# Optimization experiments

Measured on AMD Instinct MI355X. Metric: run time of the kernel, lower is better.

The kernel has to match this reference:

```python
import jax, jax.numpy as jnp
import numpy as np

N = 50000      # nodes
E = 800000     # edges (before self loops)
D_IN = 128
HID = 64
HEADS = 8
D_OUT = 10


def setup_inputs() -> dict:
    key = jax.random.key(0)
    ks = jax.random.split(key, 16)
    sc = 0.05
    x = jax.random.normal(ks[0], (N, D_IN), dtype=jnp.float32)
    edge_index = jax.random.randint(ks[1], (2, E), 0, N, dtype=jnp.int64)
    return {
        "x": x,
        "edge_index": edge_index,
        "W1": jax.random.normal(ks[2], (HEADS * HID, D_IN), dtype=jnp.float32) * sc,
        "a1_src": jax.random.normal(ks[3], (HEADS, HID), dtype=jnp.float32) * sc,
        "a1_dst": jax.random.normal(ks[4], (HEADS, HID), dtype=jnp.float32) * sc,
        "b1": jnp.zeros((HEADS * HID,), jnp.float32),
        "W2": jax.random.normal(ks[5], (HID, HEADS * HID), dtype=jnp.float32) * sc,
        "a2_src": jax.random.normal(ks[6], (1, HID), dtype=jnp.float32) * sc,
        "a2_dst": jax.random.normal(ks[7], (1, HID), dtype=jnp.float32) * sc,
        "b2": jnp.zeros((HID,), jnp.float32),
        "W3": jax.random.normal(ks[8], (HID, HID), dtype=jnp.float32) * sc,
        "a3_src": jax.random.normal(ks[9], (1, HID), dtype=jnp.float32) * sc,
        "a3_dst": jax.random.normal(ks[10], (1, HID), dtype=jnp.float32) * sc,
        "b3": jnp.zeros((HID,), jnp.float32),
        "Wc": jax.random.normal(ks[11], (D_OUT, HID), dtype=jnp.float32) * sc,
        "bc": jnp.zeros((D_OUT,), jnp.float32),
    }


def gat_conv(x, src, dst, W, a_src, a_dst, b, concat):
    """PyG GATConv (eval mode, add_self_loops already applied to src/dst)."""
    heads, out_ch = a_src.shape
    n = x.shape[0]
    h = (x @ W.T).reshape(n, heads, out_ch)          # [N, H, C]
    a_s = jnp.einsum('nhc,hc->nh', h, a_src)          # [N, H]
    a_d = jnp.einsum('nhc,hc->nh', h, a_dst)          # [N, H]
    e = jax.nn.leaky_relu(a_s[src] + a_d[dst], 0.2)   # [Etot, H]
    # segment softmax over incoming edges of each destination node
    m = jax.ops.segment_max(e, dst, num_segments=n)
    ex = jnp.exp(e - m[dst])
    s = jax.ops.segment_sum(ex, dst, num_segments=n)
    alpha = ex / (s[dst] + 1e-16)                     # [Etot, H]
    out = jax.ops.segment_sum(h[src] * alpha[:, :, None], dst, num_segments=n)
    if concat:
        out = out.reshape(n, heads * out_ch)
    else:
        out = out.mean(axis=1)
    return out + b


def reference(x, edge_index, W1, a1_src, a1_dst, b1, W2, a2_src, a2_dst, b2,
              W3, a3_src, a3_dst, b3, Wc, bc):
    loops = jnp.arange(N, dtype=edge_index.dtype)
    src = jnp.concatenate([edge_index[0], loops])
    dst = jnp.concatenate([edge_index[1], loops])
    h = jax.nn.elu(gat_conv(x, src, dst, W1, a1_src, a1_dst, b1, True))
    h = jax.nn.elu(gat_conv(h, src, dst, W2, a2_src, a2_dst, b2, False))
    h = jax.nn.elu(gat_conv(h, src, dst, W3, a3_src, a3_dst, b3, False))
    return h @ Wc.T + bc
```

## Files before the change

kernel.cpp:

```cpp
#include <hip/hip_runtime.h>
#include <math.h>

#define N_NODES 50000
#define N_EDGES 800000
#define ETOT    (N_EDGES + N_NODES)

typedef short bf16x8 __attribute__((ext_vector_type(8)));
typedef float f32x4  __attribute__((ext_vector_type(4)));

__device__ __forceinline__ float b2f(unsigned int u16) {
    return __uint_as_float(u16 << 16);
}
__device__ __forceinline__ unsigned short f2b(float f) {
    unsigned int u = __float_as_uint(f);
    u += 0x7fffu + ((u >> 16) & 1u);
    return (unsigned short)(u >> 16);
}
__device__ __forceinline__ void unpack8(uint4 v, float* f) {
    f[0] = __uint_as_float(v.x << 16); f[1] = __uint_as_float(v.x & 0xffff0000u);
    f[2] = __uint_as_float(v.y << 16); f[3] = __uint_as_float(v.y & 0xffff0000u);
    f[4] = __uint_as_float(v.z << 16); f[5] = __uint_as_float(v.z & 0xffff0000u);
    f[6] = __uint_as_float(v.w << 16); f[7] = __uint_as_float(v.w & 0xffff0000u);
}

__global__ void k_detect(const int* __restrict__ idx, int* __restrict__ flag) {
    int i = blockIdx.x * blockDim.x + threadIdx.x;
    int v = idx[2 * i + 1];
    unsigned long long any = __ballot(v != 0);
    if ((threadIdx.x & 63) == 0 && any) atomicOr(flag, 1);
}

__device__ __forceinline__ int edge_src(const int* idx, int e, int is32) {
    return is32 ? idx[e] : idx[2 * e];
}
__device__ __forceinline__ int edge_dst(const int* idx, int e, int is32) {
    return is32 ? idx[N_EDGES + e] : idx[2 * (N_EDGES + e)];
}

__global__ void k_degree(const int* __restrict__ idx, const int* __restrict__ flag,
                         int* __restrict__ deg) {
    int e = blockIdx.x * blockDim.x + threadIdx.x;
    if (e >= ETOT) return;
    int is32 = *flag;
    int d = (e < N_EDGES) ? edge_dst(idx, e, is32) : (e - N_EDGES);
    atomicAdd(&deg[d], 1);
}

__global__ __launch_bounds__(256) void k_scan1(const int* __restrict__ deg,
                                               int* __restrict__ rowptr,
                                               int* __restrict__ bsum) {
    __shared__ int sd[256];
    int t = threadIdx.x;
    int i = blockIdx.x * 256 + t;
    int v = (i < N_NODES) ? deg[i] : 0;
    sd[t] = v;
    __syncthreads();
#pragma unroll
    for (int off = 1; off < 256; off <<= 1) {
        int a = (t >= off) ? sd[t - off] : 0;
        __syncthreads();
        sd[t] += a;
        __syncthreads();
    }
    if (i < N_NODES) rowptr[i] = sd[t] - v;
    if (t == 255) bsum[blockIdx.x] = sd[255];
}

__global__ __launch_bounds__(256) void k_scan2(int* __restrict__ bsum,
                                               int* __restrict__ boff,
                                               int* __restrict__ rowptr,
                                               int nb) {
    __shared__ int sd[256];
    int t = threadIdx.x;
    int v = (t < nb) ? bsum[t] : 0;
    sd[t] = v;
    __syncthreads();
#pragma unroll
    for (int off = 1; off < 256; off <<= 1) {
        int a = (t >= off) ? sd[t - off] : 0;
        __syncthreads();
        sd[t] += a;
        __syncthreads();
    }
    boff[t] = sd[t] - v;
    if (t == 255) rowptr[N_NODES] = sd[255];
}

__global__ __launch_bounds__(256) void k_scan3(int* __restrict__ rowptr,
                                               const int* __restrict__ boff,
                                               int* __restrict__ cursor) {
    int i = blockIdx.x * 256 + threadIdx.x;
    if (i >= N_NODES) return;
    int r = rowptr[i] + boff[blockIdx.x];
    rowptr[i] = r;
    cursor[i] = r;
}

__global__ void k_scatter(const int* __restrict__ idx, const int* __restrict__ flag,
                          int* __restrict__ cursor, int* __restrict__ col) {
    int e = blockIdx.x * blockDim.x + threadIdx.x;
    if (e >= ETOT) return;
    int is32 = *flag;
    int s, d;
    if (e < N_EDGES) { s = edge_src(idx, e, is32); d = edge_dst(idx, e, is32); }
    else             { s = d = e - N_EDGES; }
    int pos = atomicAdd(&cursor[d], 1);
    col[pos] = s;
}

__global__ void k_cast_w(const float* __restrict__ w1, const float* __restrict__ w2,
                         const float* __restrict__ w3,
                         unsigned short* __restrict__ o1, unsigned short* __restrict__ o2,
                         unsigned short* __restrict__ o3) {
    int i = blockIdx.x * blockDim.x + threadIdx.x;
    if (i < 512 * 128 / 4) {
        float4 v = ((const float4*)w1)[i];
        ushort2* o = (ushort2*)(o1 + i * 4);
        o[0] = make_ushort2(f2b(v.x), f2b(v.y));
        o[1] = make_ushort2(f2b(v.z), f2b(v.w));
    }
    if (i < 64 * 512 / 4) {
        float4 v = ((const float4*)w2)[i];
        ushort2* o = (ushort2*)(o2 + i * 4);
        o[0] = make_ushort2(f2b(v.x), f2b(v.y));
        o[1] = make_ushort2(f2b(v.z), f2b(v.w));
    }
    if (i < 64 * 64 / 4) {
        float4 v = ((const float4*)w3)[i];
        ushort2* o = (ushort2*)(o3 + i * 4);
        o[0] = make_ushort2(f2b(v.x), f2b(v.y));
        o[1] = make_ushort2(f2b(v.z), f2b(v.w));
    }
}

template<int AFP32>
__global__ __launch_bounds__(256) void k_gemm(const float* __restrict__ Af,
                                              const unsigned short* __restrict__ Ab,
                                              const unsigned short* __restrict__ W,
                                              unsigned short* __restrict__ C,
                                              const float* __restrict__ a_src,
                                              const float* __restrict__ a_dst,
                                              float* __restrict__ asb,
                                              float* __restrict__ adb,
                                              int M, int K, int Nout, int Hstr) {
    __shared__ unsigned short As[64 * 40];
    __shared__ unsigned short Bs[64 * 40];
    __shared__ float red_s[4][64];
    __shared__ float red_d[4][64];
    int t = threadIdx.x;
    int w = t >> 6, l = t & 63;
    int quad = l >> 4, lm = l & 15;
    int m0 = blockIdx.y * 64, n0 = blockIdx.x * 64;
    int hd = blockIdx.x;
    int lr = t >> 2;
    int lc = (t & 3) * 8;

    f32x4 acc[4];
#pragma unroll
    for (int r = 0; r < 4; ++r) acc[r] = (f32x4){0.f, 0.f, 0.f, 0.f};

    for (int k0 = 0; k0 < K; k0 += 32) {
        int m = m0 + lr;
        if (AFP32) {
            float4 a0 = {0.f,0.f,0.f,0.f}, a1 = {0.f,0.f,0.f,0.f};
            if (m < M) {
                const float4* ap = (const float4*)(Af + (size_t)m * K + k0 + lc);
                a0 = ap[0]; a1 = ap[1];
            }
            unsigned int u0 = (unsigned int)f2b(a0.x) | ((unsigned int)f2b(a0.y) << 16);
            unsigned int u1 = (unsigned int)f2b(a0.z) | ((unsigned int)f2b(a0.w) << 16);
            unsigned int u2 = (unsigned int)f2b(a1.x) | ((unsigned int)f2b(a1.y) << 16);
            unsigned int u3 = (unsigned int)f2b(a1.z) | ((unsigned int)f2b(a1.w) << 16);
            *(uint4*)&As[lr * 40 + lc] = make_uint4(u0, u1, u2, u3);
        } else {
            uint4 av = make_uint4(0, 0, 0, 0);
            if (m < M) av = *(const uint4*)(Ab + (size_t)m * K + k0 + lc);
            *(uint4*)&As[lr * 40 + lc] = av;
        }
        uint4 bv = *(const uint4*)(W + (size_t)(n0 + lr) * K + k0 + lc);
        *(uint4*)&Bs[lr * 40 + lc] = bv;
        __syncthreads();

        bf16x8 bfrag = *(const bf16x8*)&Bs[(w * 16 + lm) * 40 + quad * 8];
#pragma unroll
        for (int r = 0; r < 4; ++r) {
            bf16x8 afrag = *(const bf16x8*)&As[(r * 16 + lm) * 40 + quad * 8];
            acc[r] = __builtin_amdgcn_mfma_f32_16x16x32_bf16(afrag, bfrag, acc[r], 0, 0, 0);
        }
        __syncthreads();
    }

#pragma unroll
    for (int r = 0; r < 4; ++r)
#pragma unroll
        for (int g = 0; g < 4; ++g) {
            int m = m0 + r * 16 + quad * 4 + g;
            if (m < M) C[(size_t)m * Nout + n0 + w * 16 + lm] = f2b(acc[r][g]);
        }

    float as = a_src[hd * 64 + w * 16 + lm];
    float ad = a_dst[hd * 64 + w * 16 + lm];
#pragma unroll
    for (int r = 0; r < 4; ++r) {
#pragma unroll
        for (int g = 0; g < 4; ++g) {
            float vs = acc[r][g] * as;
            float vd = acc[r][g] * ad;
#pragma unroll
            for (int off = 1; off < 16; off <<= 1) {
                vs += __shfl_xor(vs, off);
                vd += __shfl_xor(vd, off);
            }
            if (lm == 0) {
                red_s[w][r * 16 + quad * 4 + g] = vs;
                red_d[w][r * 16 + quad * 4 + g] = vd;
            }
        }
    }
    __syncthreads();
    if (t < 64) {
        float vs = red_s[0][t] + red_s[1][t] + red_s[2][t] + red_s[3][t];
        float vd = red_d[0][t] + red_d[1][t] + red_d[2][t] + red_d[3][t];
        int m = m0 + t;
        if (m < M) {
            asb[(size_t)m * Hstr + hd] = vs;
            adb[(size_t)m * Hstr + hd] = vd;
        }
    }
}

__global__ __launch_bounds__(256) void k_agg8(const unsigned short* __restrict__ h,
                                              const float* __restrict__ asrc,
                                              const float* __restrict__ adst,
                                              const int* __restrict__ rowptr,
                                              const int* __restrict__ col,
                                              const float* __restrict__ bias,
                                              unsigned short* __restrict__ out) {
    int n = blockIdx.x * 4 + (threadIdx.x >> 6);
    if (n >= N_NODES) return;
    int l = threadIdx.x & 63;
    int j = l >> 3;
    int start = rowptr[n], end = rowptr[n + 1];
    float adn = adst[n * 8 + j];

    float ssum = 0.f;
    float o[8] = {0.f, 0.f, 0.f, 0.f, 0.f, 0.f, 0.f, 0.f};
    int k = start;
    for (; k + 4 <= end; k += 4) {
        int s0 = col[k], s1 = col[k + 1], s2 = col[k + 2], s3 = col[k + 3];
        float t0 = asrc[s0 * 8 + j], t1 = asrc[s1 * 8 + j];
        float t2 = asrc[s2 * 8 + j], t3 = asrc[s3 * 8 + j];
        uint4 hv0 = *(const uint4*)(h + (size_t)s0 * 512 + l * 8);
        uint4 hv1 = *(const uint4*)(h + (size_t)s1 * 512 + l * 8);
        uint4 hv2 = *(const uint4*)(h + (size_t)s2 * 512 + l * 8);
        uint4 hv3 = *(const uint4*)(h + (size_t)s3 * 512 + l * 8);
        float f[8];
        float e0 = t0 + adn; e0 = (e0 > 0.f) ? e0 : 0.2f * e0;
        float ex0 = __expf(e0); ssum += ex0;
        unpack8(hv0, f);
#pragma unroll
        for (int i = 0; i < 8; ++i) o[i] += ex0 * f[i];
        float e1 = t1 + adn; e1 = (e1 > 0.f) ? e1 : 0.2f * e1;
        float ex1 = __expf(e1); ssum += ex1;
        unpack8(hv1, f);
#pragma unroll
        for (int i = 0; i < 8; ++i) o[i] += ex1 * f[i];
        float e2 = t2 + adn; e2 = (e2 > 0.f) ? e2 : 0.2f * e2;
        float ex2 = __expf(e2); ssum += ex2;
        unpack8(hv2, f);
#pragma unroll
        for (int i = 0; i < 8; ++i) o[i] += ex2 * f[i];
        float e3 = t3 + adn; e3 = (e3 > 0.f) ? e3 : 0.2f * e3;
        float ex3 = __expf(e3); ssum += ex3;
        unpack8(hv3, f);
#pragma unroll
        for (int i = 0; i < 8; ++i) o[i] += ex3 * f[i];
    }
    for (; k < end; ++k) {
        int s = col[k];
        float e = asrc[s * 8 + j] + adn;
        e = (e > 0.f) ? e : 0.2f * e;
        float ex = __expf(e);
        ssum += ex;
        uint4 hv = *(const uint4*)(h + (size_t)s * 512 + l * 8);
        float f[8];
        unpack8(hv, f);
#pragma unroll
        for (int i = 0; i < 8; ++i) o[i] += ex * f[i];
    }
    float inv = 1.f / (ssum + 1e-16f);
    unsigned int p[4];
#pragma unroll
    for (int i = 0; i < 4; ++i) {
        float v0 = o[2 * i] * inv + bias[l * 8 + 2 * i];
        float v1 = o[2 * i + 1] * inv + bias[l * 8 + 2 * i + 1];
        v0 = (v0 > 0.f) ? v0 : expm1f(v0);
        v1 = (v1 > 0.f) ? v1 : expm1f(v1);
        p[i] = (unsigned int)f2b(v0) | ((unsigned int)f2b(v1) << 16);
    }
    *(uint4*)(out + (size_t)n * 512 + l * 8) = make_uint4(p[0], p[1], p[2], p[3]);
}

__global__ __launch_bounds__(256) void k_agg1(const unsigned short* __restrict__ h,
                                              const float* __restrict__ asrc,
                                              const float* __restrict__ adst,
                                              const int* __restrict__ rowptr,
                                              const int* __restrict__ col,
                                              const float* __restrict__ bias,
                                              unsigned short* __restrict__ out,
                                              const float* __restrict__ Wc,
                                              const float* __restrict__ bc,
                                              float* __restrict__ out_cls,
                                              int cls) {
    int n = blockIdx.x * 4 + (threadIdx.x >> 6);
    if (n >= N_NODES) return;
    int l = threadIdx.x & 63;
    int start = rowptr[n], end = rowptr[n + 1];
    float adn = adst[n];

    float ssum = 0.f, o = 0.f;
    int k = start;
    for (; k + 4 <= end; k += 4) {
        int s0 = col[k], s1 = col[k + 1], s2 = col[k + 2], s3 = col[k + 3];
        float t0 = asrc[s0], t1 = asrc[s1], t2 = asrc[s2], t3 = asrc[s3];
        unsigned short q0 = h[(size_t)s0 * 64 + l];
        unsigned short q1 = h[(size_t)s1 * 64 + l];
        unsigned short q2 = h[(size_t)s2 * 64 + l];
        unsigned short q3 = h[(size_t)s3 * 64 + l];
        float e0 = t0 + adn; e0 = (e0 > 0.f) ? e0 : 0.2f * e0;
        float ex0 = __expf(e0); ssum += ex0; o += ex0 * b2f(q0);
        float e1 = t1 + adn; e1 = (e1 > 0.f) ? e1 : 0.2f * e1;
        float ex1 = __expf(e1); ssum += ex1; o += ex1 * b2f(q1);
        float e2 = t2 + adn; e2 = (e2 > 0.f) ? e2 : 0.2f * e2;
        float ex2 = __expf(e2); ssum += ex2; o += ex2 * b2f(q2);
        float e3 = t3 + adn; e3 = (e3 > 0.f) ? e3 : 0.2f * e3;
        float ex3 = __expf(e3); ssum += ex3; o += ex3 * b2f(q3);
    }
    for (; k < end; ++k) {
        int s = col[k];
        float e = asrc[s] + adn;
        e = (e > 0.f) ? e : 0.2f * e;
        float ex = __expf(e);
        ssum += ex;
        o += ex * b2f(h[(size_t)s * 64 + l]);
    }
    float v = o / (ssum + 1e-16f) + bias[l];
    v = (v > 0.f) ? v : expm1f(v);
    if (cls) {
#pragma unroll
        for (int d = 0; d < 10; ++d) {
            float p = v * Wc[d * 64 + l];
#pragma unroll
            for (int off = 32; off; off >>= 1) p += __shfl_xor(p, off);
            if (l == d) out_cls[n * 10 + d] = p + bc[d];
        }
    } else {
        out[(size_t)n * 64 + l] = f2b(v);
    }
}

extern "C" void kernel_launch(void* const* d_in, const int* in_sizes, int n_in,
                              void* d_out, int out_size, void* d_ws, size_t ws_size,
                              hipStream_t stream) {
    const float* x    = (const float*)d_in[0];
    const int*   eidx = (const int*)  d_in[1];
    const float* W1   = (const float*)d_in[2];
    const float* a1s  = (const float*)d_in[3];
    const float* a1d  = (const float*)d_in[4];
    const float* b1   = (const float*)d_in[5];
    const float* W2   = (const float*)d_in[6];
    const float* a2s  = (const float*)d_in[7];
    const float* a2d  = (const float*)d_in[8];
    const float* b2   = (const float*)d_in[9];
    const float* W3   = (const float*)d_in[10];
    const float* a3s  = (const float*)d_in[11];
    const float* a3d  = (const float*)d_in[12];
    const float* b3   = (const float*)d_in[13];
    const float* Wc   = (const float*)d_in[14];
    const float* bc   = (const float*)d_in[15];
    float* out = (float*)d_out;

    float* asbuf = (float*)d_ws;
    float* adbuf = asbuf + (size_t)N_NODES * 8;
    unsigned short* h1  = (unsigned short*)(adbuf + (size_t)N_NODES * 8);
    unsigned short* x2  = h1  + (size_t)N_NODES * 512;
    unsigned short* h2  = x2  + (size_t)N_NODES * 512;
    unsigned short* x3  = h2  + (size_t)N_NODES * 64;
    unsigned short* h3  = x3  + (size_t)N_NODES * 64;
    unsigned short* W1b = h3  + (size_t)N_NODES * 64;
    unsigned short* W2b = W1b + 512 * 128;
    unsigned short* W3b = W2b + 64 * 512;
    int* ibase  = (int*)(W3b + 64 * 64);
    int* deg    = ibase;
    int* rowptr = deg + N_NODES;
    int* cursor = rowptr + N_NODES + 1;
    int* flag   = cursor + N_NODES;
    int* bsum   = flag + 1;
    int* boff   = bsum + 256;
    int* col    = boff + 256;
    size_t int_bytes = (size_t)(N_NODES + (N_NODES + 1) + N_NODES + 1 + 512) * sizeof(int);

    hipMemsetAsync(ibase, 0, int_bytes, stream);

    dim3 blk(256);
    const int SCAN_BLOCKS = (N_NODES + 255) / 256;

    k_detect<<<32, blk, 0, stream>>>(eidx, flag);
    k_degree<<<(ETOT + 255) / 256, blk, 0, stream>>>(eidx, flag, deg);
    k_scan1<<<SCAN_BLOCKS, blk, 0, stream>>>(deg, rowptr, bsum);
    k_scan2<<<1, blk, 0, stream>>>(bsum, boff, rowptr, SCAN_BLOCKS);
    k_scan3<<<SCAN_BLOCKS, blk, 0, stream>>>(rowptr, boff, cursor);
    k_scatter<<<(ETOT + 255) / 256, blk, 0, stream>>>(eidx, flag, cursor, col);

    k_cast_w<<<64, blk, 0, stream>>>(W1, W2, W3, W1b, W2b, W3b);

    int mblocks = (N_NODES + 63) / 64;

    k_gemm<1><<<dim3(8, mblocks), blk, 0, stream>>>(x, (const unsigned short*)0, W1b, h1,
                                                    a1s, a1d, asbuf, adbuf,
                                                    N_NODES, 128, 512, 8);
    k_agg8<<<(N_NODES + 3) / 4, blk, 0, stream>>>(h1, asbuf, adbuf, rowptr, col, b1, x2);

    k_gemm<0><<<dim3(1, mblocks), blk, 0, stream>>>((const float*)0, x2, W2b, h2,
                                                    a2s, a2d, asbuf, adbuf,
                                                    N_NODES, 512, 64, 1);
    k_agg1<<<(N_NODES + 3) / 4, blk, 0, stream>>>(h2, asbuf, adbuf, rowptr, col, b2, x3,
                                                  Wc, bc, out, 0);

    k_gemm<0><<<dim3(1, mblocks), blk, 0, stream>>>((const float*)0, x3, W3b, h3,
                                                    a3s, a3d, asbuf, adbuf,
                                                    N_NODES, 64, 64, 1);
    k_agg1<<<(N_NODES + 3) / 4, blk, 0, stream>>>(h3, asbuf, adbuf, rowptr, col, b3,
                                                  (unsigned short*)0, Wc, bc, out, 1);
}
```

Before: 525.8 us.

## Fuse layer-3 GEMM into layer-2 aggregation and restructure layer-1 GEMM per row block

Layer 1's GEMM now stages a 64-row block of x into LDS once, converting it to bf16, and loops over all 8 heads, instead of re-reading and re-converting x in each of 8 head blocks. The layer-3 projection (64x64) and its attention logits are computed inside the layer-2 aggregation kernel using W3 held in LDS and wave shuffles. That removes one GEMM launch and the write and read of the intermediate x3 buffer. The memset is shrunk to cover only the degree array and flag, since the other buffers are fully overwritten. The trade-offs are fewer blocks and less parallelism for GEMM1, and extra shuffle-heavy work inside the aggregation.

```diff
diff --git a/kernel.cpp b/kernel.cpp
--- a/kernel.cpp
+++ b/kernel.cpp
@@ -133,16 +133,115 @@
     }
 }
 
-template<int AFP32>
-__global__ __launch_bounds__(256) void k_gemm(const float* __restrict__ Af,
-                                              const unsigned short* __restrict__ Ab,
+__global__ __launch_bounds__(256) void k_gemm1(const float* __restrict__ Af,
+                                               const unsigned short* __restrict__ W,
+                                               unsigned short* __restrict__ C,
+                                               const float* __restrict__ a_src,
+                                               const float* __restrict__ a_dst,
+                                               float* __restrict__ asb,
+                                               float* __restrict__ adb,
+                                               int M) {
+    __shared__ unsigned short As[64 * 136];
+    __shared__ unsigned short Bs[64 * 136];
+    __shared__ float red_s[4][64];
+    __shared__ float red_d[4][64];
+    int t = threadIdx.x;
+    int w = t >> 6, l = t & 63;
+    int quad = l >> 4, lm = l & 15;
+    int m0 = blockIdx.x * 64;
+    int lr = t >> 2;
+    int lcb = (t & 3) * 8;
+
+#pragma unroll
+    for (int seg = 0; seg < 4; ++seg) {
+        int colf = lcb + seg * 32;
+        int m = m0 + lr;
+        float4 a0 = {0.f,0.f,0.f,0.f}, a1 = {0.f,0.f,0.f,0.f};
+        if (m < M) {
+            const float4* ap = (const float4*)(Af + (size_t)m * 128 + colf);
+            a0 = ap[0]; a1 = ap[1];
+        }
+        unsigned int u0 = (unsigned int)f2b(a0.x) | ((unsigned int)f2b(a0.y) << 16);
+        unsigned int u1 = (unsigned int)f2b(a0.z) | ((unsigned int)f2b(a0.w) << 16);
+        unsigned int u2 = (unsigned int)f2b(a1.x) | ((unsigned int)f2b(a1.y) << 16);
+        unsigned int u3 = (unsigned int)f2b(a1.z) | ((unsigned int)f2b(a1.w) << 16);
+        *(uint4*)&As[lr * 136 + colf] = make_uint4(u0, u1, u2, u3);
+    }
+    __syncthreads();
+
+    for (int hd = 0; hd < 8; ++hd) {
+#pragma unroll
+        for (int seg = 0; seg < 4; ++seg) {
+            int colf = lcb + seg * 32;
+            uint4 bv = *(const uint4*)(W + (size_t)(hd * 64 + lr) * 128 + colf);
+            *(uint4*)&Bs[lr * 136 + colf] = bv;
+        }
+        __syncthreads();
+
+        f32x4 acc[4];
+#pragma unroll
+        for (int r = 0; r < 4; ++r) acc[r] = (f32x4){0.f, 0.f, 0.f, 0.f};
+
+#pragma unroll
+        for (int k0 = 0; k0 < 4; ++k0) {
+            int koff = k0 * 32 + quad * 8;
+            bf16x8 bfrag = *(const bf16x8*)&Bs[(w * 16 + lm) * 136 + koff];
+#pragma unroll
+            for (int r = 0; r < 4; ++r) {
+                bf16x8 afrag = *(const bf16x8*)&As[(r * 16 + lm) * 136 + koff];
+                acc[r] = __builtin_amdgcn_mfma_f32_16x16x32_bf16(afrag, bfrag, acc[r], 0, 0, 0);
+            }
+        }
+
+#pragma unroll
+        for (int r = 0; r < 4; ++r)
+#pragma unroll
+            for (int g = 0; g < 4; ++g) {
+                int m = m0 + r * 16 + quad * 4 + g;
+                if (m < M) C[(size_t)m * 512 + hd * 64 + w * 16 + lm] = f2b(acc[r][g]);
+            }
+
+        float as = a_src[hd * 64 + w * 16 + lm];
+        float ad = a_dst[hd * 64 + w * 16 + lm];
+#pragma unroll
+        for (int r = 0; r < 4; ++r) {
+#pragma unroll
+            for (int g = 0; g < 4; ++g) {
+                float vs = acc[r][g] * as;
+                float vd = acc[r][g] * ad;
+#pragma unroll
+                for (int off = 1; off < 16; off <<= 1) {
+                    vs += __shfl_xor(vs, off);
+                    vd += __shfl_xor(vd, off);
+                }
+                if (lm == 0) {
+                    red_s[w][r * 16 + quad * 4 + g] = vs;
+                    red_d[w][r * 16 + quad * 4 + g] = vd;
+                }
+            }
+        }
+        __syncthreads();
+        if (t < 64) {
+            float vs = red_s[0][t] + red_s[1][t] + red_s[2][t] + red_s[3][t];
+            float vd = red_d[0][t] + red_d[1][t] + red_d[2][t] + red_d[3][t];
+            int m = m0 + t;
+            if (m < M) {
+                asb[(size_t)m * 8 + hd] = vs;
+                adb[(size_t)m * 8 + hd] = vd;
+            }
+        }
+        __syncthreads();
+    }
+}
+
+__global__ __launch_bounds__(256) void k_gemm(const unsigned short* __restrict__ A,
                                               const unsigned short* __restrict__ W,
                                               unsigned short* __restrict__ C,
                                               const float* __restrict__ a_src,
                                               const float* __restrict__ a_dst,
                                               float* __restrict__ asb,
                                               float* __restrict__ adb,
-                                              int M, int K, int Nout, int Hstr) {
+                                              int M, int K) {
     __shared__ unsigned short As[64 * 40];
     __shared__ unsigned short Bs[64 * 40];
     __shared__ float red_s[4][64];
@@ -150,8 +249,7 @@
     int t = threadIdx.x;
     int w = t >> 6, l = t & 63;
     int quad = l >> 4, lm = l & 15;
-    int m0 = blockIdx.y * 64, n0 = blockIdx.x * 64;
-    int hd = blockIdx.x;
+    int m0 = blockIdx.y * 64;
     int lr = t >> 2;
     int lc = (t & 3) * 8;
 
@@ -161,23 +259,10 @@
 
     for (int k0 = 0; k0 < K; k0 += 32) {
         int m = m0 + lr;
-        if (AFP32) {
-            float4 a0 = {0.f,0.f,0.f,0.f}, a1 = {0.f,0.f,0.f,0.f};
-            if (m < M) {
-                const float4* ap = (const float4*)(Af + (size_t)m * K + k0 + lc);
-                a0 = ap[0]; a1 = ap[1];
-            }
-            unsigned int u0 = (unsigned int)f2b(a0.x) | ((unsigned int)f2b(a0.y) << 16);
-            unsigned int u1 = (unsigned int)f2b(a0.z) | ((unsigned int)f2b(a0.w) << 16);
-            unsigned int u2 = (unsigned int)f2b(a1.x) | ((unsigned int)f2b(a1.y) << 16);
-            unsigned int u3 = (unsigned int)f2b(a1.z) | ((unsigned int)f2b(a1.w) << 16);
-            *(uint4*)&As[lr * 40 + lc] = make_uint4(u0, u1, u2, u3);
-        } else {
-            uint4 av = make_uint4(0, 0, 0, 0);
-            if (m < M) av = *(const uint4*)(Ab + (size_t)m * K + k0 + lc);
-            *(uint4*)&As[lr * 40 + lc] = av;
-        }
-        uint4 bv = *(const uint4*)(W + (size_t)(n0 + lr) * K + k0 + lc);
+        uint4 av = make_uint4(0, 0, 0, 0);
+        if (m < M) av = *(const uint4*)(A + (size_t)m * K + k0 + lc);
+        *(uint4*)&As[lr * 40 + lc] = av;
+        uint4 bv = *(const uint4*)(W + (size_t)lr * K + k0 + lc);
         *(uint4*)&Bs[lr * 40 + lc] = bv;
         __syncthreads();
 
@@ -195,11 +280,11 @@
 #pragma unroll
         for (int g = 0; g < 4; ++g) {
             int m = m0 + r * 16 + quad * 4 + g;
-            if (m < M) C[(size_t)m * Nout + n0 + w * 16 + lm] = f2b(acc[r][g]);
-        }
-
-    float as = a_src[hd * 64 + w * 16 + lm];
-    float ad = a_dst[hd * 64 + w * 16 + lm];
+            if (m < M) C[(size_t)m * 64 + w * 16 + lm] = f2b(acc[r][g]);
+        }
+
+    float as = a_src[w * 16 + lm];
+    float ad = a_dst[w * 16 + lm];
 #pragma unroll
     for (int r = 0; r < 4; ++r) {
 #pragma unroll
@@ -223,8 +308,8 @@
         float vd = red_d[0][t] + red_d[1][t] + red_d[2][t] + red_d[3][t];
         int m = m0 + t;
         if (m < M) {
-            asb[(size_t)m * Hstr + hd] = vs;
-            adb[(size_t)m * Hstr + hd] = vd;
+            asb[m] = vs;
+            adb[m] = vd;
         }
     }
 }
@@ -301,20 +386,29 @@
     *(uint4*)(out + (size_t)n * 512 + l * 8) = make_uint4(p[0], p[1], p[2], p[3]);
 }
 
-__global__ __launch_bounds__(256) void k_agg1(const unsigned short* __restrict__ h,
-                                              const float* __restrict__ asrc,
-                                              const float* __restrict__ adst,
-                                              const int* __restrict__ rowptr,
-                                              const int* __restrict__ col,
-                                              const float* __restrict__ bias,
-                                              unsigned short* __restrict__ out,
-                                              const float* __restrict__ Wc,
-                                              const float* __restrict__ bc,
-                                              float* __restrict__ out_cls,
-                                              int cls) {
-    int n = blockIdx.x * 4 + (threadIdx.x >> 6);
-    if (n >= N_NODES) return;
-    int l = threadIdx.x & 63;
+__global__ __launch_bounds__(256) void k_agg1_mid(const unsigned short* __restrict__ h,
+                                                  const float* __restrict__ asrc,
+                                                  const float* __restrict__ adst,
+                                                  const int* __restrict__ rowptr,
+                                                  const int* __restrict__ col,
+                                                  const float* __restrict__ bias,
+                                                  const unsigned short* __restrict__ W3b,
+                                                  const float* __restrict__ a3s,
+                                                  const float* __restrict__ a3d,
+                                                  unsigned short* __restrict__ h3,
+                                                  float* __restrict__ as2,
+                                                  float* __restrict__ ad2) {
+    __shared__ unsigned short sW3[64 * 68];
+    int t = threadIdx.x;
+    {
+        int r0 = t >> 2, c0 = (t & 3) * 16;
+        *(uint4*)&sW3[r0 * 68 + c0]     = *(const uint4*)(W3b + r0 * 64 + c0);
+        *(uint4*)&sW3[r0 * 68 + c0 + 8] = *(const uint4*)(W3b + r0 * 64 + c0 + 8);
+    }
+    __syncthreads();
+
+    int n = blockIdx.x * 4 + (t >> 6);
+    int l = t & 63;
     int start = rowptr[n], end = rowptr[n + 1];
     float adn = adst[n];
 
@@ -346,16 +440,78 @@
     }
     float v = o / (ssum + 1e-16f) + bias[l];
     v = (v > 0.f) ? v : expm1f(v);
-    if (cls) {
-#pragma unroll
-        for (int d = 0; d < 10; ++d) {
-            float p = v * Wc[d * 64 + l];
-#pragma unroll
-            for (int off = 32; off; off >>= 1) p += __shfl_xor(p, off);
-            if (l == d) out_cls[n * 10 + d] = p + bc[d];
-        }
-    } else {
-        out[(size_t)n * 64 + l] = f2b(v);
+
+    float acc3 = 0.f;
+#pragma unroll
+    for (int cb = 0; cb < 8; ++cb) {
+        uint4 wv = *(const uint4*)&sW3[l * 68 + cb * 8];
+        float wf[8];
+        unpack8(wv, wf);
+#pragma unroll
+        for (int i = 0; i < 8; ++i)
+            acc3 += __shfl(v, cb * 8 + i) * wf[i];
+    }
+
+    float ps = acc3 * a3s[l];
+    float pd = acc3 * a3d[l];
+#pragma unroll
+    for (int off = 32; off; off >>= 1) {
+        ps += __shfl_xor(ps, off);
+        pd += __shfl_xor(pd, off);
+    }
+    if (l == 0) { as2[n] = ps; ad2[n] = pd; }
+    h3[(size_t)n * 64 + l] = f2b(acc3);
+}
+
+__global__ __launch_bounds__(256) void k_agg1_cls(const unsigned short* __restrict__ h,
+                                                  const float* __restrict__ asrc,
+                                                  const float* __restrict__ adst,
+                                                  const int* __restrict__ rowptr,
+                                                  const int* __restrict__ col,
+                                                  const float* __restrict__ bias,
+                                                  const float* __restrict__ Wc,
+                                                  const float* __restrict__ bc,
+                                                  float* __restrict__ out_cls) {
+    int n = blockIdx.x * 4 + (threadIdx.x >> 6);
+    if (n >= N_NODES) return;
+    int l = threadIdx.x & 63;
+    int start = rowptr[n], end = rowptr[n + 1];
+    float adn = adst[n];
+
+    float ssum = 0.f, o = 0.f;
+    int k = start;
+    for (; k + 4 <= end; k += 4) {
+        int s0 = col[k], s1 = col[k + 1], s2 = col[k + 2], s3 = col[k + 3];
+        float t0 = asrc[s0], t1 = asrc[s1], t2 = asrc[s2], t3 = asrc[s3];
+        unsigned short q0 = h[(size_t)s0 * 64 + l];
+        unsigned short q1 = h[(size_t)s1 * 64 + l];
+        unsigned short q2 = h[(size_t)s2 * 64 + l];
+        unsigned short q3 = h[(size_t)s3 * 64 + l];
+        float e0 = t0 + adn; e0 = (e0 > 0.f) ? e0 : 0.2f * e0;
+        float ex0 = __expf(e0); ssum += ex0; o += ex0 * b2f(q0);
+        float e1 = t1 + adn; e1 = (e1 > 0.f) ? e1 : 0.2f * e1;
+        float ex1 = __expf(e1); ssum += ex1; o += ex1 * b2f(q1);
+        float e2 = t2 + adn; e2 = (e2 > 0.f) ? e2 : 0.2f * e2;
+        float ex2 = __expf(e2); ssum += ex2; o += ex2 * b2f(q2);
+        float e3 = t3 + adn; e3 = (e3 > 0.f) ? e3 : 0.2f * e3;
+        float ex3 = __expf(e3); ssum += ex3; o += ex3 * b2f(q3);
+    }
+    for (; k < end; ++k) {
+        int s = col[k];
+        float e = asrc[s] + adn;
+        e = (e > 0.f) ? e : 0.2f * e;
+        float ex = __expf(e);
+        ssum += ex;
+        o += ex * b2f(h[(size_t)s * 64 + l]);
+    }
+    float v = o / (ssum + 1e-16f) + bias[l];
+    v = (v > 0.f) ? v : expm1f(v);
+#pragma unroll
+    for (int d = 0; d < 10; ++d) {
+        float p = v * Wc[d * 64 + l];
+#pragma unroll
+        for (int off = 32; off; off >>= 1) p += __shfl_xor(p, off);
+        if (l == d) out_cls[n * 10 + d] = p + bc[d];
     }
 }
 
@@ -382,25 +538,26 @@
 
     float* asbuf = (float*)d_ws;
     float* adbuf = asbuf + (size_t)N_NODES * 8;
-    unsigned short* h1  = (unsigned short*)(adbuf + (size_t)N_NODES * 8);
+    float* as2   = adbuf + (size_t)N_NODES * 8;
+    float* ad2   = as2 + N_NODES;
+    unsigned short* h1  = (unsigned short*)(ad2 + N_NODES);
     unsigned short* x2  = h1  + (size_t)N_NODES * 512;
     unsigned short* h2  = x2  + (size_t)N_NODES * 512;
-    unsigned short* x3  = h2  + (size_t)N_NODES * 64;
-    unsigned short* h3  = x3  + (size_t)N_NODES * 64;
+    unsigned short* h3  = h2  + (size_t)N_NODES * 64;
     unsigned short* W1b = h3  + (size_t)N_NODES * 64;
     unsigned short* W2b = W1b + 512 * 128;
     unsigned short* W3b = W2b + 64 * 512;
     int* ibase  = (int*)(W3b + 64 * 64);
     int* deg    = ibase;
-    int* rowptr = deg + N_NODES;
+    int* flag   = deg + N_NODES;
+    int* rowptr = flag + 1;
     int* cursor = rowptr + N_NODES + 1;
-    int* flag   = cursor + N_NODES;
-    int* bsum   = flag + 1;
+    int* bsum   = cursor + N_NODES;
     int* boff   = bsum + 256;
     int* col    = boff + 256;
-    size_t int_bytes = (size_t)(N_NODES + (N_NODES + 1) + N_NODES + 1 + 512) * sizeof(int);
-
-    hipMemsetAsync(ibase, 0, int_bytes, stream);
+    size_t memset_bytes = (size_t)(N_NODES + 1) * sizeof(int);
+
+    hipMemsetAsync(ibase, 0, memset_bytes, stream);
 
     dim3 blk(256);
     const int SCAN_BLOCKS = (N_NODES + 255) / 256;
@@ -415,21 +572,15 @@
     k_cast_w<<<64, blk, 0, stream>>>(W1, W2, W3, W1b, W2b, W3b);
 
     int mblocks = (N_NODES + 63) / 64;
-
-    k_gemm<1><<<dim3(8, mblocks), blk, 0, stream>>>(x, (const unsigned short*)0, W1b, h1,
-                                                    a1s, a1d, asbuf, adbuf,
-                                                    N_NODES, 128, 512, 8);
-    k_agg8<<<(N_NODES + 3) / 4, blk, 0, stream>>>(h1, asbuf, adbuf, rowptr, col, b1, x2);
-
-    k_gemm<0><<<dim3(1, mblocks), blk, 0, stream>>>((const float*)0, x2, W2b, h2,
-                                                    a2s, a2d, asbuf, adbuf,
-                                                    N_NODES, 512, 64, 1);
-    k_agg1<<<(N_NODES + 3) / 4, blk, 0, stream>>>(h2, asbuf, adbuf, rowptr, col, b2, x3,
-                                                  Wc, bc, out, 0);
-
-    k_gemm<0><<<dim3(1, mblocks), blk, 0, stream>>>((const float*)0, x3, W3b, h3,
-                                                    a3s, a3d, asbuf, adbuf,
-                                                    N_NODES, 64, 64, 1);
-    k_agg1<<<(N_NODES + 3) / 4, blk, 0, stream>>>(h3, asbuf, adbuf, rowptr, col, b3,
-                                                  (unsigned short*)0, Wc, bc, out, 1);
-}
+    int nblocks = N_NODES / 4;
+
+    k_gemm1<<<mblocks, blk, 0, stream>>>(x, W1b, h1, a1s, a1d, asbuf, adbuf, N_NODES);
+    k_agg8<<<nblocks, blk, 0, stream>>>(h1, asbuf, adbuf, rowptr, col, b1, x2);
+
+    k_gemm<<<dim3(1, mblocks), blk, 0, stream>>>(x2, W2b, h2, a2s, a2d, asbuf, adbuf,
+                                                 N_NODES, 512);
+    k_agg1_mid<<<nblocks, blk, 0, stream>>>(h2, asbuf, adbuf, rowptr, col, b2,
+                                            W3b, a3s, a3d, h3, as2, ad2);
+
+    k_agg1_cls<<<nblocks, blk, 0, stream>>>(h3, as2, ad2, rowptr, col, b3, Wc, bc, out);
+}
```

Result: slower. 564.2 us (+7.3%).

## Fuse layer-3 linear transform and attention scores into layer-2 aggregation

Applied to the files above, without the earlier changes.

The layer-3 GEMM is folded into the layer-2 aggregation kernel. Each wavefront multiplies its aggregated 64-wide node vector by W3, held in shared memory, using lane shuffles, then computes the src/dst attention scores and writes h3 directly. This removes a kernel launch and the write and re-read of the intermediate x3 buffer. The memset is also shrunk to cover only the degree array and flag, after reordering the workspace layout. New separate as2/ad2 buffers avoid a race with asbuf, which the fused kernel is still reading.

```diff
diff --git a/kernel.cpp b/kernel.cpp
--- a/kernel.cpp
+++ b/kernel.cpp
@@ -301,20 +301,29 @@
     *(uint4*)(out + (size_t)n * 512 + l * 8) = make_uint4(p[0], p[1], p[2], p[3]);
 }
 
-__global__ __launch_bounds__(256) void k_agg1(const unsigned short* __restrict__ h,
-                                              const float* __restrict__ asrc,
-                                              const float* __restrict__ adst,
-                                              const int* __restrict__ rowptr,
-                                              const int* __restrict__ col,
-                                              const float* __restrict__ bias,
-                                              unsigned short* __restrict__ out,
-                                              const float* __restrict__ Wc,
-                                              const float* __restrict__ bc,
-                                              float* __restrict__ out_cls,
-                                              int cls) {
-    int n = blockIdx.x * 4 + (threadIdx.x >> 6);
-    if (n >= N_NODES) return;
-    int l = threadIdx.x & 63;
+__global__ __launch_bounds__(256) void k_agg1_mid(const unsigned short* __restrict__ h,
+                                                  const float* __restrict__ asrc,
+                                                  const float* __restrict__ adst,
+                                                  const int* __restrict__ rowptr,
+                                                  const int* __restrict__ col,
+                                                  const float* __restrict__ bias,
+                                                  const unsigned short* __restrict__ W3b,
+                                                  const float* __restrict__ a3s,
+                                                  const float* __restrict__ a3d,
+                                                  unsigned short* __restrict__ h3,
+                                                  float* __restrict__ as2,
+                                                  float* __restrict__ ad2) {
+    __shared__ unsigned short sW3[64 * 68];
+    int t = threadIdx.x;
+    {
+        int r0 = t >> 2, c0 = (t & 3) * 16;
+        *(uint4*)&sW3[r0 * 68 + c0]     = *(const uint4*)(W3b + r0 * 64 + c0);
+        *(uint4*)&sW3[r0 * 68 + c0 + 8] = *(const uint4*)(W3b + r0 * 64 + c0 + 8);
+    }
+    __syncthreads();
+
+    int n = blockIdx.x * 4 + (t >> 6);
+    int l = t & 63;
     int start = rowptr[n], end = rowptr[n + 1];
     float adn = adst[n];
 
@@ -346,16 +355,78 @@
     }
     float v = o / (ssum + 1e-16f) + bias[l];
     v = (v > 0.f) ? v : expm1f(v);
-    if (cls) {
-#pragma unroll
-        for (int d = 0; d < 10; ++d) {
-            float p = v * Wc[d * 64 + l];
-#pragma unroll
-            for (int off = 32; off; off >>= 1) p += __shfl_xor(p, off);
-            if (l == d) out_cls[n * 10 + d] = p + bc[d];
-        }
-    } else {
-        out[(size_t)n * 64 + l] = f2b(v);
+
+    float acc3 = 0.f;
+#pragma unroll
+    for (int cb = 0; cb < 8; ++cb) {
+        uint4 wv = *(const uint4*)&sW3[l * 68 + cb * 8];
+        float wf[8];
+        unpack8(wv, wf);
+#pragma unroll
+        for (int i = 0; i < 8; ++i)
+            acc3 += __shfl(v, cb * 8 + i) * wf[i];
+    }
+
+    float ps = acc3 * a3s[l];
+    float pd = acc3 * a3d[l];
+#pragma unroll
+    for (int off = 32; off; off >>= 1) {
+        ps += __shfl_xor(ps, off);
+        pd += __shfl_xor(pd, off);
+    }
+    if (l == 0) { as2[n] = ps; ad2[n] = pd; }
+    h3[(size_t)n * 64 + l] = f2b(acc3);
+}
+
+__global__ __launch_bounds__(256) void k_agg1_cls(const unsigned short* __restrict__ h,
+                                                  const float* __restrict__ asrc,
+                                                  const float* __restrict__ adst,
+                                                  const int* __restrict__ rowptr,
+                                                  const int* __restrict__ col,
+                                                  const float* __restrict__ bias,
+                                                  const float* __restrict__ Wc,
+                                                  const float* __restrict__ bc,
+                                                  float* __restrict__ out_cls) {
+    int n = blockIdx.x * 4 + (threadIdx.x >> 6);
+    if (n >= N_NODES) return;
+    int l = threadIdx.x & 63;
+    int start = rowptr[n], end = rowptr[n + 1];
+    float adn = adst[n];
+
+    float ssum = 0.f, o = 0.f;
+    int k = start;
+    for (; k + 4 <= end; k += 4) {
+        int s0 = col[k], s1 = col[k + 1], s2 = col[k + 2], s3 = col[k + 3];
+        float t0 = asrc[s0], t1 = asrc[s1], t2 = asrc[s2], t3 = asrc[s3];
+        unsigned short q0 = h[(size_t)s0 * 64 + l];
+        unsigned short q1 = h[(size_t)s1 * 64 + l];
+        unsigned short q2 = h[(size_t)s2 * 64 + l];
+        unsigned short q3 = h[(size_t)s3 * 64 + l];
+        float e0 = t0 + adn; e0 = (e0 > 0.f) ? e0 : 0.2f * e0;
+        float ex0 = __expf(e0); ssum += ex0; o += ex0 * b2f(q0);
+        float e1 = t1 + adn; e1 = (e1 > 0.f) ? e1 : 0.2f * e1;
+        float ex1 = __expf(e1); ssum += ex1; o += ex1 * b2f(q1);
+        float e2 = t2 + adn; e2 = (e2 > 0.f) ? e2 : 0.2f * e2;
+        float ex2 = __expf(e2); ssum += ex2; o += ex2 * b2f(q2);
+        float e3 = t3 + adn; e3 = (e3 > 0.f) ? e3 : 0.2f * e3;
+        float ex3 = __expf(e3); ssum += ex3; o += ex3 * b2f(q3);
+    }
+    for (; k < end; ++k) {
+        int s = col[k];
+        float e = asrc[s] + adn;
+        e = (e > 0.f) ? e : 0.2f * e;
+        float ex = __expf(e);
+        ssum += ex;
+        o += ex * b2f(h[(size_t)s * 64 + l]);
+    }
+    float v = o / (ssum + 1e-16f) + bias[l];
+    v = (v > 0.f) ? v : expm1f(v);
+#pragma unroll
+    for (int d = 0; d < 10; ++d) {
+        float p = v * Wc[d * 64 + l];
+#pragma unroll
+        for (int off = 32; off; off >>= 1) p += __shfl_xor(p, off);
+        if (l == d) out_cls[n * 10 + d] = p + bc[d];
     }
 }
 
@@ -382,25 +453,26 @@
 
     float* asbuf = (float*)d_ws;
     float* adbuf = asbuf + (size_t)N_NODES * 8;
-    unsigned short* h1  = (unsigned short*)(adbuf + (size_t)N_NODES * 8);
+    float* as2   = adbuf + (size_t)N_NODES * 8;
+    float* ad2   = as2 + N_NODES;
+    unsigned short* h1  = (unsigned short*)(ad2 + N_NODES);
     unsigned short* x2  = h1  + (size_t)N_NODES * 512;
     unsigned short* h2  = x2  + (size_t)N_NODES * 512;
-    unsigned short* x3  = h2  + (size_t)N_NODES * 64;
-    unsigned short* h3  = x3  + (size_t)N_NODES * 64;
+    unsigned short* h3  = h2  + (size_t)N_NODES * 64;
     unsigned short* W1b = h3  + (size_t)N_NODES * 64;
     unsigned short* W2b = W1b + 512 * 128;
     unsigned short* W3b = W2b + 64 * 512;
     int* ibase  = (int*)(W3b + 64 * 64);
     int* deg    = ibase;
-    int* rowptr = deg + N_NODES;
+    int* flag   = deg + N_NODES;
+    int* rowptr = flag + 1;
     int* cursor = rowptr + N_NODES + 1;
-    int* flag   = cursor + N_NODES;
-    int* bsum   = flag + 1;
+    int* bsum   = cursor + N_NODES;
     int* boff   = bsum + 256;
     int* col    = boff + 256;
-    size_t int_bytes = (size_t)(N_NODES + (N_NODES + 1) + N_NODES + 1 + 512) * sizeof(int);
-
-    hipMemsetAsync(ibase, 0, int_bytes, stream);
+    size_t memset_bytes = (size_t)(N_NODES + 1) * sizeof(int);
+
+    hipMemsetAsync(ibase, 0, memset_bytes, stream);
 
     dim3 blk(256);
     const int SCAN_BLOCKS = (N_NODES + 255) / 256;
@@ -415,21 +487,18 @@
     k_cast_w<<<64, blk, 0, stream>>>(W1, W2, W3, W1b, W2b, W3b);
 
     int mblocks = (N_NODES + 63) / 64;
+    int nblocks = N_NODES / 4;
 
     k_gemm<1><<<dim3(8, mblocks), blk, 0, stream>>>(x, (const unsigned short*)0, W1b, h1,
                                                     a1s, a1d, asbuf, adbuf,
                                                     N_NODES, 128, 512, 8);
-    k_agg8<<<(N_NODES + 3) / 4, blk, 0, stream>>>(h1, asbuf, adbuf, rowptr, col, b1, x2);
+    k_agg8<<<nblocks, blk, 0, stream>>>(h1, asbuf, adbuf, rowptr, col, b1, x2);
 
     k_gemm<0><<<dim3(1, mblocks), blk, 0, stream>>>((const float*)0, x2, W2b, h2,
                                                     a2s, a2d, asbuf, adbuf,
                                                     N_NODES, 512, 64, 1);
-    k_agg1<<<(N_NODES + 3) / 4, blk, 0, stream>>>(h2, asbuf, adbuf, rowptr, col, b2, x3,
-                                                  Wc, bc, out, 0);
-
-    k_gemm<0><<<dim3(1, mblocks), blk, 0, stream>>>((const float*)0, x3, W3b, h3,
-                                                    a3s, a3d, asbuf, adbuf,
-                                                    N_NODES, 64, 64, 1);
-    k_agg1<<<(N_NODES + 3) / 4, blk, 0, stream>>>(h3, asbuf, adbuf, rowptr, col, b3,
-                                                  (unsigned short*)0, Wc, bc, out, 1);
-}
+    k_agg1_mid<<<nblocks, blk, 0, stream>>>(h2, asbuf, adbuf, rowptr, col, b2,
+                                            W3b, a3s, a3d, h3, as2, ad2);
+
+    k_agg1_cls<<<nblocks, blk, 0, stream>>>(h3, as2, ad2, rowptr, col, b3, Wc, bc, out);
+}
```

Result: slower. 547.9 us (+4.2%).
